# Kernel tuning notes

Measured on AMD Instinct MI355X. Metric: run time of the kernel, lower is better.

Reference implementation:

```python
import jax, jax.numpy as jnp
import numpy as np

N_NODES = 100000
N_EDGES = 800000
HIDDEN = 128


def setup_inputs() -> dict:
    key = jax.random.key(0)
    k1, k2, k3, k4, k5, k6 = jax.random.split(key, 6)
    z = jax.random.normal(k1, (N_NODES, HIDDEN), dtype=jnp.float32)
    edge_index = jax.random.randint(k2, (2, N_EDGES), 0, N_NODES, dtype=jnp.int64)
    # nn.Linear params (torch default init scale ~ 1/sqrt(fan_in))
    s1 = 1.0 / np.sqrt(2 * HIDDEN)
    s2 = 1.0 / np.sqrt(HIDDEN)
    W1 = jax.random.uniform(k3, (2 * HIDDEN, HIDDEN), jnp.float32, -s1, s1)
    b1 = jax.random.uniform(k4, (HIDDEN,), jnp.float32, -s1, s1)
    W2 = jax.random.uniform(k5, (HIDDEN, 1), jnp.float32, -s2, s2)
    b2 = jax.random.uniform(k6, (1,), jnp.float32, -s2, s2)
    return {"z": z, "edge_index": edge_index, "W1": W1, "b1": b1, "W2": W2, "b2": b2}


def reference(z, edge_index, W1, b1, W2, b2):
    src, dst = edge_index[0], edge_index[1]
    # Gather endpoint features: [E, H] each. Avoid materializing the [E, 2H]
    # concat by splitting W1 into src/dst halves (same math as cat + matmul).
    W1_src, W1_dst = W1[:HIDDEN], W1[HIDDEN:]
    h = z[src] @ W1_src + z[dst] @ W1_dst + b1  # [E, H]
    h = jax.nn.relu(h)
    score = h @ W2 + b2  # [E, 1]
    return score
```

## Files before the change

kernel.cpp:

```cpp
#include <hip/hip_runtime.h>
#include <hip/hip_bf16.h>

#define N_NODES 100000
#define N_EDGES 800000
#define HIDDEN 128
#define N_TILES 1563
#define PC_GRID 512

typedef short frag_ab __attribute__((ext_vector_type(8)));
typedef float frag_cd __attribute__((ext_vector_type(4)));

__device__ inline unsigned short f2b(float f) {
    union { float f; unsigned u; } x; x.f = f;
    return (unsigned short)((x.u + 0x7fffu + ((x.u >> 16) & 1u)) >> 16);
}

__device__ inline unsigned pk2(float x, float y) {
    union { __hip_bfloat162 h; unsigned u; } c;
    c.h = __float22bfloat162_rn(make_float2(x, y));
    return c.u;
}

__global__ __launch_bounds__(256) void transpose_w1(
    const float* __restrict__ W1, unsigned short* __restrict__ Bt)
{
    const int t  = threadIdx.x;
    const int nc = blockIdx.x * 4 + (t >> 6);
    const int k2 = (t & 63) * 2;
    const int col  = nc & 127;
    const int roff = (nc >= 128) ? 128 : 0;
    float f0 = W1[(size_t)(roff + k2)     * HIDDEN + col];
    float f1 = W1[(size_t)(roff + k2 + 1) * HIDDEN + col];
    *(unsigned*)(Bt + (size_t)nc * HIDDEN + k2) = (unsigned)f2b(f0) | ((unsigned)f2b(f1) << 16);
}

#define AS_STRIDE 136
#define CS_STRIDE 264

__global__ __launch_bounds__(256) void precompute_uv_mfma(
    const float* __restrict__ z, const unsigned short* __restrict__ Bt,
    const float* __restrict__ b1, unsigned short* __restrict__ UV)
{
    __shared__ unsigned short smem[64 * CS_STRIDE];
    const int t = threadIdx.x;
    const int lane = t & 63;
    const int w = t >> 6;
    const int wn = w * 64;
    const int g  = lane >> 4;
    const int lc = lane & 15;

    frag_ab b[4][4];
    float bias[4];
    #pragma unroll
    for (int nt = 0; nt < 4; ++nt) {
        int nc = wn + nt * 16 + lc;
        bias[nt] = (nc < HIDDEN) ? b1[nc] : 0.f;
        const unsigned short* brow = Bt + (size_t)nc * HIDDEN;
        #pragma unroll
        for (int q = 0; q < 4; ++q)
            b[nt][q] = *(const frag_ab*)(brow + q * 32 + g * 8);
    }

    int tile = blockIdx.x;
    uint2 pf[8];
    #pragma unroll
    for (int i = 0; i < 8; ++i) {
        int f4 = i * 256 + t;
        int m = tile * 64 + (f4 >> 5);
        if (m >= N_NODES) m = N_NODES - 1;
        float4 v = ((const float4*)z)[(size_t)m * 32 + (f4 & 31)];
        pf[i].x = pk2(v.x, v.y);
        pf[i].y = pk2(v.z, v.w);
    }

    while (true) {
        #pragma unroll
        for (int i = 0; i < 8; ++i) {
            int f4 = i * 256 + t;
            *(uint2*)&smem[(f4 >> 5) * AS_STRIDE + (f4 & 31) * 4] = pf[i];
        }
        __syncthreads();

        const int next = tile + PC_GRID;
        const bool have_next = (next < N_TILES);
        if (have_next) {
            #pragma unroll
            for (int i = 0; i < 8; ++i) {
                int f4 = i * 256 + t;
                int m = next * 64 + (f4 >> 5);
                if (m >= N_NODES) m = N_NODES - 1;
                float4 v = ((const float4*)z)[(size_t)m * 32 + (f4 & 31)];
                pf[i].x = pk2(v.x, v.y);
                pf[i].y = pk2(v.z, v.w);
            }
        }

        frag_cd acc[4][4];
        #pragma unroll
        for (int mt = 0; mt < 4; ++mt)
            #pragma unroll
            for (int nt = 0; nt < 4; ++nt)
                acc[mt][nt] = (frag_cd){0.f, 0.f, 0.f, 0.f};
        #pragma unroll
        for (int q = 0; q < 4; ++q) {
            frag_ab a[4];
            #pragma unroll
            for (int mt = 0; mt < 4; ++mt)
                a[mt] = *(const frag_ab*)&smem[(mt * 16 + lc) * AS_STRIDE + q * 32 + g * 8];
            #pragma unroll
            for (int mt = 0; mt < 4; ++mt)
                #pragma unroll
                for (int nt = 0; nt < 4; ++nt)
                    acc[mt][nt] = __builtin_amdgcn_mfma_f32_16x16x32_bf16(
                        a[mt], b[nt][q], acc[mt][nt], 0, 0, 0);
        }
        __syncthreads();

        #pragma unroll
        for (int nt = 0; nt < 4; ++nt) {
            int nc = wn + nt * 16 + lc;
            #pragma unroll
            for (int mt = 0; mt < 4; ++mt)
                #pragma unroll
                for (int r = 0; r < 4; ++r)
                    smem[(mt * 16 + g * 4 + r) * CS_STRIDE + nc] =
                        f2b(acc[mt][nt][r] + bias[nt]);
        }
        __syncthreads();

        const int m0 = tile * 64;
        #pragma unroll
        for (int i = 0; i < 8; ++i) {
            int f = i * 256 + t;
            int m = f >> 5;
            int c16 = f & 31;
            if (m0 + m < N_NODES) {
                uint4 val = *(const uint4*)&smem[m * CS_STRIDE + c16 * 8];
                *(uint4*)&UV[(size_t)(m0 + m) * 256 + c16 * 8] = val;
            }
        }
        if (!have_next) break;
        __syncthreads();
        tile = next;
    }
}

__device__ inline float2 bf2(unsigned u) {
    union { unsigned i; float f; } lo, hi;
    lo.i = u << 16;
    hi.i = u & 0xffff0000u;
    return make_float2(lo.f, hi.f);
}

__device__ inline float2 rfma2(unsigned u, unsigned v, float2 w, float2 acc) {
    float2 uf = bf2(u), vf = bf2(v);
    float2 s = make_float2(uf.x + vf.x, uf.y + vf.y);
    s.x = fmaxf(s.x, 0.f); s.y = fmaxf(s.y, 0.f);
    acc.x = __builtin_fmaf(s.x, w.x, acc.x);
    acc.y = __builtin_fmaf(s.y, w.y, acc.y);
    return acc;
}

__global__ __launch_bounds__(256) void edge_score(
    const int* __restrict__ ei, const unsigned short* __restrict__ UV,
    const float* __restrict__ W2, const float* __restrict__ B2,
    float* __restrict__ out)
{
    const int t = threadIdx.x;
    const int g = t & 7;
    const int slot = t >> 3;
    const int e0 = blockIdx.x * 64 + slot;
    const int e1 = e0 + 32;

    const float4* W24 = (const float4*)W2;
    const float4 w0 = W24[g * 4 + 0];
    const float4 w1 = W24[g * 4 + 1];
    const float4 w2 = W24[g * 4 + 2];
    const float4 w3 = W24[g * 4 + 3];

    const int s0 = ei[e0];
    const int d0 = ei[N_EDGES + e0];
    const int s1 = ei[e1];
    const int d1 = ei[N_EDGES + e1];

    const uint4* u0p = (const uint4*)(UV + (size_t)s0 * 256) + g * 2;
    const uint4* v0p = (const uint4*)(UV + (size_t)d0 * 256 + 128) + g * 2;
    const uint4* u1p = (const uint4*)(UV + (size_t)s1 * 256) + g * 2;
    const uint4* v1p = (const uint4*)(UV + (size_t)d1 * 256 + 128) + g * 2;
    const uint4 ua0 = u0p[0], ub0 = u0p[1];
    const uint4 va0 = v0p[0], vb0 = v0p[1];
    const uint4 ua1 = u1p[0], ub1 = u1p[1];
    const uint4 va1 = v1p[0], vb1 = v1p[1];

    float2 A = make_float2(0.f, 0.f), B = make_float2(0.f, 0.f);
    A = rfma2(ua0.x, va0.x, make_float2(w0.x, w0.y), A);
    A = rfma2(ua0.y, va0.y, make_float2(w0.z, w0.w), A);
    A = rfma2(ua0.z, va0.z, make_float2(w1.x, w1.y), A);
    A = rfma2(ua0.w, va0.w, make_float2(w1.z, w1.w), A);
    A = rfma2(ub0.x, vb0.x, make_float2(w2.x, w2.y), A);
    A = rfma2(ub0.y, vb0.y, make_float2(w2.z, w2.w), A);
    A = rfma2(ub0.z, vb0.z, make_float2(w3.x, w3.y), A);
    A = rfma2(ub0.w, vb0.w, make_float2(w3.z, w3.w), A);

    B = rfma2(ua1.x, va1.x, make_float2(w0.x, w0.y), B);
    B = rfma2(ua1.y, va1.y, make_float2(w0.z, w0.w), B);
    B = rfma2(ua1.z, va1.z, make_float2(w1.x, w1.y), B);
    B = rfma2(ua1.w, va1.w, make_float2(w1.z, w1.w), B);
    B = rfma2(ub1.x, vb1.x, make_float2(w2.x, w2.y), B);
    B = rfma2(ub1.y, vb1.y, make_float2(w2.z, w2.w), B);
    B = rfma2(ub1.z, vb1.z, make_float2(w3.x, w3.y), B);
    B = rfma2(ub1.w, vb1.w, make_float2(w3.z, w3.w), B);

    float sa = A.x + A.y;
    float sb = B.x + B.y;
    sa += __shfl_xor(sa, 1, 8);
    sa += __shfl_xor(sa, 2, 8);
    sa += __shfl_xor(sa, 4, 8);
    sb += __shfl_xor(sb, 1, 8);
    sb += __shfl_xor(sb, 2, 8);
    sb += __shfl_xor(sb, 4, 8);

    if (g == 0) {
        float bb = B2[0];
        out[e0] = sa + bb;
        out[e1] = sb + bb;
    }
}

extern "C" void kernel_launch(void* const* d_in, const int* in_sizes, int n_in,
                              void* d_out, int out_size, void* d_ws, size_t ws_size,
                              hipStream_t stream) {
    const float* z  = (const float*)d_in[0];
    const int*   ei = (const int*)d_in[1];
    const float* W1 = (const float*)d_in[2];
    const float* b1 = (const float*)d_in[3];
    const float* W2 = (const float*)d_in[4];
    const float* b2 = (const float*)d_in[5];
    float* out = (float*)d_out;

    unsigned short* UV = (unsigned short*)d_ws;
    unsigned short* Bt = UV + (size_t)N_NODES * 256;

    transpose_w1<<<64, 256, 0, stream>>>(W1, Bt);
    precompute_uv_mfma<<<PC_GRID, 256, 0, stream>>>(z, Bt, b1, UV);
    edge_score<<<N_EDGES / 64, 256, 0, stream>>>(ei, UV, W2, b2, out);
}
```

Before: 163.5 us.

## Pre-swizzle z into MFMA fragment layout in a separate kernel

Adds a kernel that converts z to bf16 and writes it into a workspace buffer already arranged in MFMA A-fragment order. A new one-tile-per-block GEMM kernel reads those fragments straight from global memory, with no LDS staging or software prefetch loop. The path runs only if the workspace is large enough, otherwise the old kernel is used. It adds an extra launch and a full write and read of a bf16 copy of z, which costs more memory traffic than the fused conversion it replaces.

```diff
diff --git a/kernel.cpp b/kernel.cpp
--- a/kernel.cpp
+++ b/kernel.cpp
@@ -34,8 +34,114 @@
     *(unsigned*)(Bt + (size_t)nc * HIDDEN + k2) = (unsigned)f2b(f0) | ((unsigned)f2b(f1) << 16);
 }
 
+__global__ __launch_bounds__(256) void zswz(
+    const float* __restrict__ z, uint4* __restrict__ zf)
+{
+    __shared__ unsigned short s[64 * 136];
+    const int t = threadIdx.x;
+    const int r0 = blockIdx.x * 64;
+
+    #pragma unroll
+    for (int i = 0; i < 8; ++i) {
+        int f4 = i * 256 + t;
+        int m = f4 >> 5;
+        int c4 = f4 & 31;
+        int mr = r0 + m; if (mr >= N_NODES) mr = N_NODES - 1;
+        float4 v = ((const float4*)z)[(size_t)mr * 32 + c4];
+        uint2 p;
+        p.x = pk2(v.x, v.y);
+        p.y = pk2(v.z, v.w);
+        *(uint2*)&s[m * 136 + c4 * 4] = p;
+    }
+    __syncthreads();
+
+    const int q = t >> 6;
+    const int l = t & 63;
+    const int g = l >> 4;
+    const int lc = l & 15;
+    #pragma unroll
+    for (int i = 0; i < 4; ++i) {
+        int row = i * 16 + lc;
+        uint4 chunk = *(const uint4*)&s[row * 136 + q * 32 + g * 8];
+        zf[((size_t)(blockIdx.x * 4 + i) * 4 + q) * 64 + l] = chunk;
+    }
+}
+
+#define CS_STRIDE 264
+
+__global__ __launch_bounds__(256) void precompute_uv_mfma_v2(
+    const uint4* __restrict__ zf, const unsigned short* __restrict__ Bt,
+    const float* __restrict__ b1, unsigned short* __restrict__ UV)
+{
+    __shared__ unsigned short smem[64 * CS_STRIDE];
+    const int t = threadIdx.x;
+    const int lane = t & 63;
+    const int w = t >> 6;
+    const int wn = w * 64;
+    const int g  = lane >> 4;
+    const int lc = lane & 15;
+    const int tile = blockIdx.x;
+
+    frag_ab b[4][4];
+    float bias[4];
+    #pragma unroll
+    for (int nt = 0; nt < 4; ++nt) {
+        int nc = wn + nt * 16 + lc;
+        bias[nt] = (nc < HIDDEN) ? b1[nc] : 0.f;
+        const unsigned short* brow = Bt + (size_t)nc * HIDDEN;
+        #pragma unroll
+        for (int q = 0; q < 4; ++q)
+            b[nt][q] = *(const frag_ab*)(brow + q * 32 + g * 8);
+    }
+
+    frag_cd acc[4][4];
+    #pragma unroll
+    for (int mt = 0; mt < 4; ++mt)
+        #pragma unroll
+        for (int nt = 0; nt < 4; ++nt)
+            acc[mt][nt] = (frag_cd){0.f, 0.f, 0.f, 0.f};
+
+    const frag_ab* zfa = (const frag_ab*)zf;
+    #pragma unroll
+    for (int q = 0; q < 4; ++q) {
+        frag_ab a[4];
+        #pragma unroll
+        for (int mt = 0; mt < 4; ++mt)
+            a[mt] = zfa[((size_t)(tile * 4 + mt) * 4 + q) * 64 + lane];
+        #pragma unroll
+        for (int mt = 0; mt < 4; ++mt)
+            #pragma unroll
+            for (int nt = 0; nt < 4; ++nt)
+                acc[mt][nt] = __builtin_amdgcn_mfma_f32_16x16x32_bf16(
+                    a[mt], b[nt][q], acc[mt][nt], 0, 0, 0);
+    }
+
+    #pragma unroll
+    for (int nt = 0; nt < 4; ++nt) {
+        int nc = wn + nt * 16 + lc;
+        #pragma unroll
+        for (int mt = 0; mt < 4; ++mt)
+            #pragma unroll
+            for (int r = 0; r < 4; ++r)
+                smem[(mt * 16 + g * 4 + r) * CS_STRIDE + nc] =
+                    f2b(acc[mt][nt][r] + bias[nt]);
+    }
+    __syncthreads();
+
+    const int m0 = tile * 64;
+    #pragma unroll
+    for (int i = 0; i < 8; ++i) {
+        int f = i * 256 + t;
+        int m = f >> 5;
+        int c16 = f & 31;
+        if (m0 + m < N_NODES) {
+            uint4 val = *(const uint4*)&smem[m * CS_STRIDE + c16 * 8];
+            *(uint4*)&UV[(size_t)(m0 + m) * 256 + c16 * 8] = val;
+        }
+    }
+}
+
 #define AS_STRIDE 136
-#define CS_STRIDE 264
 
 __global__ __launch_bounds__(256) void precompute_uv_mfma(
     const float* __restrict__ z, const unsigned short* __restrict__ Bt,
@@ -240,8 +346,18 @@
 
     unsigned short* UV = (unsigned short*)d_ws;
     unsigned short* Bt = UV + (size_t)N_NODES * 256;
+    uint4* zf = (uint4*)(Bt + (size_t)256 * HIDDEN);
+
+    const size_t need = (size_t)N_NODES * 256 * 2
+                      + (size_t)256 * HIDDEN * 2
+                      + (size_t)N_TILES * 4 * 4 * 64 * 16;
 
     transpose_w1<<<64, 256, 0, stream>>>(W1, Bt);
-    precompute_uv_mfma<<<PC_GRID, 256, 0, stream>>>(z, Bt, b1, UV);
+    if (ws_size >= need) {
+        zswz<<<N_TILES, 256, 0, stream>>>(z, zf);
+        precompute_uv_mfma_v2<<<N_TILES, 256, 0, stream>>>(zf, Bt, b1, UV);
+    } else {
+        precompute_uv_mfma<<<PC_GRID, 256, 0, stream>>>(z, Bt, b1, UV);
+    }
     edge_score<<<N_EDGES / 64, 256, 0, stream>>>(ei, UV, W2, b2, out);
 }
```

Measured after the change: 180.1 us. 1.1x slower.
